# Optimization experiments

Measured on AMD Instinct MI355X. Metric: run time of the kernel, lower is better.

Reference implementation:

```python
import jax, jax.numpy as jnp
import numpy as np

B, T, E, H = 4, 2048, 1024, 16
D = E // H  # head_dim = 64
THETA = 10000.0


def setup_inputs() -> dict:
    key = jax.random.key(0)
    ks = jax.random.split(key, 3)
    s = 0.02
    return {
        "x": jax.random.normal(ks[0], (B, T, E), jnp.float32),
        "W_attn": jax.random.normal(ks[1], (E, 3 * E), jnp.float32) * s,
        "b_attn": jnp.zeros((3 * E,), jnp.float32),
        "W_proj": jax.random.normal(ks[2], (E, E), jnp.float32) * s,
        "b_proj": jnp.zeros((E,), jnp.float32),
    }


def _rope(x, position_offset=0):
    # x: (B, H, T, D) -- interleaved even/odd pair rotation, as in apply_rope
    t, d = x.shape[2], x.shape[3]
    pos = jnp.arange(position_offset, position_offset + t, dtype=jnp.float32)
    inv_freq = 1.0 / (THETA ** (jnp.arange(0, d, 2, dtype=jnp.float32) / d))
    freqs = jnp.outer(pos, inv_freq)  # (T, D/2)
    cos = jnp.cos(freqs)[None, None].astype(x.dtype)
    sin = jnp.sin(freqs)[None, None].astype(x.dtype)
    xe = x[..., ::2]
    xo = x[..., 1::2]
    rot = jnp.stack((xe * cos - xo * sin, xe * sin + xo * cos), axis=-1)
    return rot.reshape(x.shape)


def reference(x, W_attn, b_attn, W_proj, b_proj):
    # fused qkv projection
    qkv = x @ W_attn + b_attn  # (B, T, 3E)
    q, k, v = jnp.split(qkv, 3, axis=-1)

    def heads(a):
        return a.reshape(B, T, H, D).transpose(0, 2, 1, 3)  # (B,H,T,D)

    q, k, v = heads(q), heads(k), heads(v)
    q = _rope(q)
    k = _rope(k)

    scores = jnp.einsum('bhqd,bhkd->bhqk', q, k) * (D ** -0.5)  # (B,H,T,T)
    causal = jnp.tril(jnp.ones((T, T), dtype=bool))
    scores = jnp.where(causal[None, None], scores, -jnp.inf)
    weights = jax.nn.softmax(scores, axis=-1)  # dropout p=0 (eval) -> identity

    out = jnp.einsum('bhqk,bhkd->bhqd', weights, v)
    out = out.transpose(0, 2, 1, 3).reshape(B, T, E)
    return out @ W_proj + b_proj
```

## Files before the change

kernel.cpp:

```cpp
#include <hip/hip_runtime.h>
#include <hip/hip_bf16.h>
#include <math.h>

#define TT 2048
#define HH 16

typedef short s16x8 __attribute__((ext_vector_type(8)));
typedef float f32x4 __attribute__((ext_vector_type(4)));

#define F4(p) (*reinterpret_cast<const float4*>(p))

__device__ __forceinline__ void gload16(const void* g, void* l) {
    __builtin_amdgcn_global_load_lds(
        (const __attribute__((address_space(1))) void*)g,
        (__attribute__((address_space(3))) void*)l, 16, 0, 0);
}

__device__ __forceinline__ ushort bf1(float a) {
    __hip_bfloat16 h = __float2bfloat16(a);
    union { __hip_bfloat16 h1; ushort u; } c; c.h1 = h; return c.u;
}
__device__ __forceinline__ uint pack_bf2(float a, float b) {
    __hip_bfloat162 h = __float22bfloat162_rn(make_float2(a, b));
    union { __hip_bfloat162 h2; uint u; } c; c.h2 = h; return c.u;
}

__global__ __launch_bounds__(256) void prep_kernel(
    const float* __restrict__ x, const float* __restrict__ Wa,
    const float* __restrict__ Wp, ushort* __restrict__ xb,
    ushort* __restrict__ wat, ushort* __restrict__ wpt, float2* __restrict__ cs)
{
    __shared__ float tsh[64][65];
    const int blk = blockIdx.x;
    const int tid = threadIdx.x;

    if (blk < 256) {
        int idx = blk * 256 + tid;
        int t = idx >> 5;
        int i = idx & 31;
        double inv_d = exp(((double)(-2 * i) / 64.0) * log(10000.0));
        float invf = (float)inv_d;
        float freq = (float)t * invf;
        double df = (double)freq;
        cs[idx] = make_float2((float)cos(df), (float)sin(df));
    } else if (blk < 4352) {
        size_t i = (size_t)(blk - 256) * 2048 + (size_t)tid * 8;
        float4 a = F4(&x[i]); float4 b = F4(&x[i + 4]);
        s16x8 v;
        v[0] = bf1(a.x); v[1] = bf1(a.y); v[2] = bf1(a.z); v[3] = bf1(a.w);
        v[4] = bf1(b.x); v[5] = bf1(b.y); v[6] = bf1(b.z); v[7] = bf1(b.w);
        *reinterpret_cast<s16x8*>(&xb[i]) = v;
    } else {
        const float* in; ushort* out; int R, C, bx, by;
        if (blk < 5120) { int r = blk - 4352; in = Wa; out = wat; R = 1024; C = 3072; bx = r % 48; by = r / 48; }
        else            { int r = blk - 5120; in = Wp; out = wpt; R = 1024; C = 1024; bx = r & 15; by = r >> 4; }
        int r0 = by * 64, c0 = bx * 64;
        int ix = tid & 15, iy = tid >> 4;
#pragma unroll
        for (int j = 0; j < 4; ++j) {
            float4 v = F4(&in[(size_t)(r0 + iy + j * 16) * C + c0 + ix * 4]);
            tsh[iy + j * 16][ix * 4 + 0] = v.x;
            tsh[iy + j * 16][ix * 4 + 1] = v.y;
            tsh[iy + j * 16][ix * 4 + 2] = v.z;
            tsh[iy + j * 16][ix * 4 + 3] = v.w;
        }
        __syncthreads();
        int oc = tid >> 2, seg = tid & 3;
        s16x8 u0, u1;
#pragma unroll
        for (int i = 0; i < 8; ++i) u0[i] = bf1(tsh[seg * 16 + i][oc]);
#pragma unroll
        for (int i = 0; i < 8; ++i) u1[i] = bf1(tsh[seg * 16 + 8 + i][oc]);
        ushort* dst = &out[(size_t)(c0 + oc) * R + r0 + seg * 16];
        *reinterpret_cast<s16x8*>(dst) = u0;
        *reinterpret_cast<s16x8*>(dst + 8) = u1;
    }
}

__global__ __launch_bounds__(256, 2) void qkv_gemm_kernel(
    const ushort* __restrict__ xb,
    const ushort* __restrict__ wat,
    const float* __restrict__ bias,
    const float2* __restrict__ cs,
    ushort* __restrict__ qg, ushort* __restrict__ kg, ushort* __restrict__ vt)
{
    __shared__ ushort As[2][8192];
    __shared__ ushort Bs[2][8192];

    const int tid = threadIdx.x;
    const int lane = tid & 63, wid = tid >> 6;
    const int lane15 = lane & 15, kgrp = lane >> 4;
    const int wr = wid >> 1, wc = wid & 1;
    const int m0 = blockIdx.y * 128, n0 = blockIdx.x * 128;
    const int swz = (lane15 & 7) << 4;
    const int srcsw = ((lane & 7) ^ ((lane >> 3) & 7)) * 8;
    const int kgrp16 = kgrp * 16;
    const float SCL = 0.125f * 1.44269504088896f;

    f32x4 acc[4][4] = {};

#define STAGE_QKV(bufi, kofs)                                                     \
    do {                                                                          \
        _Pragma("unroll")                                                         \
        for (int i_ = 0; i_ < 4; ++i_) {                                          \
            int c_ = wid * 4 + i_;                                                \
            gload16(xb + (size_t)(m0 + c_ * 8 + (lane >> 3)) * 1024 + (kofs) + srcsw, \
                    &As[bufi][c_ * 512]);                                         \
            gload16(wat + (size_t)(n0 + c_ * 8 + (lane >> 3)) * 1024 + (kofs) + srcsw, \
                    &Bs[bufi][c_ * 512]);                                         \
        }                                                                         \
    } while (0)

    STAGE_QKV(0, 0);
    int buf = 0;
    for (int kt = 0; kt < 16; ++kt) {
        __syncthreads();
        if (kt < 15) STAGE_QKV(buf ^ 1, (kt + 1) * 64);
        const char* Ap = (const char*)As[buf];
        const char* Bp = (const char*)Bs[buf];
#pragma unroll
        for (int ks = 0; ks < 2; ++ks) {
            s16x8 af[4], bfv[4];
            const int kb = (ks * 64 + kgrp16) ^ swz;
#pragma unroll
            for (int f = 0; f < 4; ++f) {
                int row = wr * 64 + f * 16 + lane15;
                af[f] = *reinterpret_cast<const s16x8*>(Ap + row * 128 + kb);
            }
#pragma unroll
            for (int g = 0; g < 4; ++g) {
                int row = wc * 64 + g * 16 + lane15;
                bfv[g] = *reinterpret_cast<const s16x8*>(Bp + row * 128 + kb);
            }
            __builtin_amdgcn_s_setprio(1);
#pragma unroll
            for (int f = 0; f < 4; ++f)
#pragma unroll
                for (int g = 0; g < 4; ++g)
                    acc[f][g] = __builtin_amdgcn_mfma_f32_16x16x32_bf16(
                        af[f], bfv[g], acc[f][g], 0, 0, 0);
            __builtin_amdgcn_s_setprio(0);
        }
        buf ^= 1;
    }

#pragma unroll
    for (int g = 0; g < 4; ++g) {
        const int n = n0 + wc * 64 + g * 16 + lane15;
        const int sec = n >> 10;
        const int e = n & 1023;
        const int hh = e >> 6, d = e & 63;
        const float bsv = bias[n];
#pragma unroll
        for (int f = 0; f < 4; ++f) {
            const int mb = m0 + wr * 64 + f * 16 + kgrp * 4;
            const int bb = mb >> 11;
            const int t0 = mb & 2047;
            if (sec == 2) {
                float v0 = acc[f][g][0] + bsv, v1 = acc[f][g][1] + bsv;
                float v2 = acc[f][g][2] + bsv, v3 = acc[f][g][3] + bsv;
                uint2 u = make_uint2(pack_bf2(v0, v1), pack_bf2(v2, v3));
                *reinterpret_cast<uint2*>(
                    &vt[((size_t)(bb * HH + hh) * 64 + d) * TT + t0]) = u;
            } else {
                ushort* dst = (sec == 0) ? qg : kg;
#pragma unroll
                for (int r = 0; r < 4; ++r) {
                    float v = acc[f][g][r] + bsv;
                    float p = __shfl_xor(v, 1);
                    float2 c2 = cs[(t0 + r) * 32 + (d >> 1)];
                    float rv = (d & 1) ? (p * c2.y + v * c2.x) : (v * c2.x - p * c2.y);
                    if (sec == 0) rv *= SCL;
                    dst[((size_t)(bb * HH + hh) * TT + t0 + r) * 64 + d] = bf1(rv);
                }
            }
        }
    }
#undef STAGE_QKV
}

__global__ __launch_bounds__(512, 6) void flash_kernel(
    const ushort* __restrict__ qg, const ushort* __restrict__ kg,
    const ushort* __restrict__ vt, ushort* __restrict__ aob)
{
    __shared__ ushort K_s[2][4096];
    __shared__ ushort V_s[2][4096];
    __shared__ ushort P_s[8192];

    const int tid = threadIdx.x;
    const int lane = tid & 63, wid = tid >> 6;
    const int lane15 = lane & 15, kgrp = lane >> 4;
    const int j = blockIdx.x;
    const int qt = 15 - (j >> 6);
    const int bh = j & 63;
    const int b = bh >> 4, h = bh & 15;
    const int q0 = qt * 128;
    const int wq = wid * 16;
    const int wq_abs = q0 + wq;
    const int swz = (lane15 & 7) << 4;
    const int srcsw = ((lane & 7) ^ ((lane >> 3) & 7)) * 8;
    const int kgrp16 = kgrp * 16;
    const int nt = 2 * qt + 2;

    const ushort* qp = qg + (size_t)bh * TT * 64;
    const ushort* kp = kg + (size_t)bh * TT * 64;
    const ushort* vp = vt + (size_t)bh * 64 * TT;
    char* Pw = (char*)P_s + wid * 2048;

#define STAGE_KV(bufi, kv0_)                                                      \
    do {                                                                          \
        gload16(kp + (size_t)((kv0_) + wid * 8 + (lane >> 3)) * 64 + srcsw,       \
                &K_s[bufi][wid * 512]);                                           \
        gload16(vp + (size_t)(wid * 8 + (lane >> 3)) * TT + (kv0_) + srcsw,       \
                &V_s[bufi][wid * 512]);                                           \
    } while (0)

    const ushort* qrow = qp + (size_t)(q0 + wq + lane15) * 64 + kgrp * 8;
    s16x8 qfr[2];
    qfr[0] = *reinterpret_cast<const s16x8*>(qrow);
    qfr[1] = *reinterpret_cast<const s16x8*>(qrow + 32);

    STAGE_KV(0, 0);

    f32x4 o[4] = {};
    float mreg = -3.0e38f;
    float lreg = 0.f;

    int buf = 0;
    for (int t = 0; t < nt; ++t) {
        __syncthreads();
        if (t + 1 < nt) STAGE_KV(buf ^ 1, (t + 1) * 64);

        const int kv0 = t * 64;
        if (kv0 <= wq_abs + 15) {
            const char* Kp = (const char*)K_s[buf];
            const char* Vp = (const char*)V_s[buf];

            f32x4 sacc[4] = {};
#pragma unroll
            for (int ks = 0; ks < 2; ++ks) {
                const int kb = (ks * 64 + kgrp16) ^ swz;
                s16x8 ka[4];
#pragma unroll
                for (int kf = 0; kf < 4; ++kf)
                    ka[kf] = *reinterpret_cast<const s16x8*>(Kp + (kf * 16 + lane15) * 128 + kb);
                __builtin_amdgcn_s_setprio(1);
#pragma unroll
                for (int kf = 0; kf < 4; ++kf)
                    sacc[kf] = __builtin_amdgcn_mfma_f32_16x16x32_bf16(
                        ka[kf], qfr[ks], sacc[kf], 0, 0, 0);
                __builtin_amdgcn_s_setprio(0);
            }

            const int qglob = q0 + wq + lane15;
            const bool masked = (kv0 + 63 > wq_abs);
            float mx = -3.0e38f;
            if (masked) {
#pragma unroll
                for (int kf = 0; kf < 4; ++kf)
#pragma unroll
                    for (int r = 0; r < 4; ++r) {
                        int kvg = kv0 + kf * 16 + kgrp * 4 + r;
                        float v = (kvg > qglob) ? -3.0e38f : sacc[kf][r];
                        sacc[kf][r] = v;
                        mx = fmaxf(mx, v);
                    }
            } else {
#pragma unroll
                for (int kf = 0; kf < 4; ++kf)
#pragma unroll
                    for (int r = 0; r < 4; ++r) mx = fmaxf(mx, sacc[kf][r]);
            }
            mx = fmaxf(mx, __shfl_xor(mx, 16));
            mx = fmaxf(mx, __shfl_xor(mx, 32));
            if (!__all(mx <= mreg + 8.f)) {
                const float mnew = fmaxf(mreg, mx);
                const float fs = exp2f(mreg - mnew);
                lreg *= fs;
#pragma unroll
                for (int df = 0; df < 4; ++df) o[df] *= fs;
                mreg = mnew;
            }
            float rsum = 0.f;
#pragma unroll
            for (int kf = 0; kf < 4; ++kf) {
                float p0 = exp2f(sacc[kf][0] - mreg);
                float p1 = exp2f(sacc[kf][1] - mreg);
                float p2 = exp2f(sacc[kf][2] - mreg);
                float p3 = exp2f(sacc[kf][3] - mreg);
                rsum += (p0 + p1) + (p2 + p3);
                uint2 u = make_uint2(pack_bf2(p0, p1), pack_bf2(p2, p3));
                int kvb = (kf * 32 + kgrp * 8) ^ swz;
                *reinterpret_cast<uint2*>(Pw + lane15 * 128 + kvb) = u;
            }
            rsum += __shfl_xor(rsum, 16);
            rsum += __shfl_xor(rsum, 32);
            lreg += rsum;

#pragma unroll
            for (int ks = 0; ks < 2; ++ks) {
                const int kb = (ks * 64 + kgrp16) ^ swz;
                s16x8 va[4], pb;
#pragma unroll
                for (int df = 0; df < 4; ++df)
                    va[df] = *reinterpret_cast<const s16x8*>(Vp + (df * 16 + lane15) * 128 + kb);
                pb = *reinterpret_cast<const s16x8*>(Pw + lane15 * 128 + kb);
                __builtin_amdgcn_s_setprio(1);
#pragma unroll
                for (int df = 0; df < 4; ++df)
                    o[df] = __builtin_amdgcn_mfma_f32_16x16x32_bf16(
                        va[df], pb, o[df], 0, 0, 0);
                __builtin_amdgcn_s_setprio(0);
            }
        }
        buf ^= 1;
    }

    {
        const float inv = 1.0f / lreg;
        const int row = wq + lane15;
#pragma unroll
        for (int df = 0; df < 4; ++df) {
            float p0 = o[df][0] * inv, p1 = o[df][1] * inv;
            float p2 = o[df][2] * inv, p3 = o[df][3] * inv;
            uint2 u = make_uint2(pack_bf2(p0, p1), pack_bf2(p2, p3));
            int db = (df * 32 + kgrp * 8) ^ ((row & 7) << 4);
            *reinterpret_cast<uint2*>((char*)P_s + row * 128 + db) = u;
        }
    }
    __syncthreads();
    {
        const int q = tid >> 2, seg = tid & 3;
        ushort* orow = aob + ((size_t)(b * TT + q0 + q)) * 1024 + h * 64 + seg * 16;
        int p0 = (seg * 32) ^ ((q & 7) << 4);
        int p1 = (seg * 32 + 16) ^ ((q & 7) << 4);
        s16x8 v0 = *reinterpret_cast<const s16x8*>((const char*)P_s + q * 128 + p0);
        s16x8 v1 = *reinterpret_cast<const s16x8*>((const char*)P_s + q * 128 + p1);
        *reinterpret_cast<s16x8*>(orow) = v0;
        *reinterpret_cast<s16x8*>(orow + 8) = v1;
    }
#undef STAGE_KV
}

__global__ __launch_bounds__(256, 2) void proj_gemm_kernel(
    const ushort* __restrict__ ab,
    const ushort* __restrict__ wpt,
    const float* __restrict__ bias,
    float* __restrict__ out)
{
    __shared__ ushort As[2][8192];
    __shared__ ushort Bs[2][8192];

    const int tid = threadIdx.x;
    const int lane = tid & 63, wid = tid >> 6;
    const int lane15 = lane & 15, kgrp = lane >> 4;
    const int wr = wid >> 1, wc = wid & 1;
    const int m0 = blockIdx.y * 128, n0 = blockIdx.x * 128;
    const int swz = (lane15 & 7) << 4;
    const int srcsw = ((lane & 7) ^ ((lane >> 3) & 7)) * 8;
    const int kgrp16 = kgrp * 16;

    f32x4 acc[4][4] = {};

#define STAGE_PRJ(bufi, kofs)                                                     \
    do {                                                                          \
        _Pragma("unroll")                                                         \
        for (int i_ = 0; i_ < 4; ++i_) {                                          \
            int c_ = wid * 4 + i_;                                                \
            gload16(ab + (size_t)(m0 + c_ * 8 + (lane >> 3)) * 1024 + (kofs) + srcsw, \
                    &As[bufi][c_ * 512]);                                         \
            gload16(wpt + (size_t)(n0 + c_ * 8 + (lane >> 3)) * 1024 + (kofs) + srcsw, \
                    &Bs[bufi][c_ * 512]);                                         \
        }                                                                         \
    } while (0)

    STAGE_PRJ(0, 0);
    int buf = 0;
    for (int kt = 0; kt < 16; ++kt) {
        __syncthreads();
        if (kt < 15) STAGE_PRJ(buf ^ 1, (kt + 1) * 64);
        const char* Ap = (const char*)As[buf];
        const char* Bp = (const char*)Bs[buf];
#pragma unroll
        for (int ks = 0; ks < 2; ++ks) {
            s16x8 af[4], bfv[4];
            const int kb = (ks * 64 + kgrp16) ^ swz;
#pragma unroll
            for (int f = 0; f < 4; ++f) {
                int row = wr * 64 + f * 16 + lane15;
                af[f] = *reinterpret_cast<const s16x8*>(Ap + row * 128 + kb);
            }
#pragma unroll
            for (int g = 0; g < 4; ++g) {
                int row = wc * 64 + g * 16 + lane15;
                bfv[g] = *reinterpret_cast<const s16x8*>(Bp + row * 128 + kb);
            }
            __builtin_amdgcn_s_setprio(1);
#pragma unroll
            for (int f = 0; f < 4; ++f)
#pragma unroll
                for (int g = 0; g < 4; ++g)
                    acc[f][g] = __builtin_amdgcn_mfma_f32_16x16x32_bf16(
                        af[f], bfv[g], acc[f][g], 0, 0, 0);
            __builtin_amdgcn_s_setprio(0);
        }
        buf ^= 1;
    }

#pragma unroll
    for (int g = 0; g < 4; ++g) {
        const int n = n0 + wc * 64 + g * 16 + lane15;
        const float bv = bias[n];
#pragma unroll
        for (int f = 0; f < 4; ++f)
#pragma unroll
            for (int r = 0; r < 4; ++r) {
                const int m = m0 + wr * 64 + f * 16 + kgrp * 4 + r;
                out[(size_t)m * 1024 + n] = acc[f][g][r] + bv;
            }
    }
#undef STAGE_PRJ
}

extern "C" void kernel_launch(void* const* d_in, const int* in_sizes, int n_in,
                              void* d_out, int out_size, void* d_ws, size_t ws_size,
                              hipStream_t stream) {
    const float* x  = (const float*)d_in[0];
    const float* Wa = (const float*)d_in[1];
    const float* ba = (const float*)d_in[2];
    const float* Wp = (const float*)d_in[3];
    const float* bp = (const float*)d_in[4];
    float* out = (float*)d_out;

    char* ws = (char*)d_ws;
    ushort* xb  = (ushort*)(ws + 0);
    ushort* wat = (ushort*)(ws + 16777216);
    ushort* wpt = (ushort*)(ws + 23068672);
    ushort* qg  = (ushort*)(ws + 25165824);
    ushort* kg  = (ushort*)(ws + 41943040);
    ushort* vtg = (ushort*)(ws + 58720256);
    ushort* aob = (ushort*)(ws + 75497472);
    float2* cs  = (float2*)(ws + 92274688);

    prep_kernel<<<dim3(5376), dim3(256), 0, stream>>>(x, Wa, Wp, xb, wat, wpt, cs);
    qkv_gemm_kernel<<<dim3(24, 64), dim3(256), 0, stream>>>(xb, wat, ba, cs, qg, kg, vtg);
    flash_kernel<<<dim3(1024), dim3(512), 0, stream>>>(qg, kg, vtg, aob);
    proj_gemm_kernel<<<dim3(8, 64), dim3(256), 0, stream>>>(aob, wpt, bp, out);
}
```

Measured before the change: 270.3 us.

## Compute softmax row sums via MFMA, use raw exp2, remap GEMM blocks per XCD

In the flash kernel, the per-row sum of probabilities is now taken from an extra MFMA against a vector of bf16 ones, replacing the shuffle reductions. The row max is computed with a balanced fmax tree after the masking step, and exp2f is replaced with the raw hardware v_exp_f32 instruction. Both GEMM kernels switch to a 1D grid whose block indices are remapped so consecutive tiles land on the same XCD, which should improve L2 reuse. The ones-MFMA adds matrix work per tile and sums the bf16-rounded probabilities, so the normalisation changes slightly in precision.

```diff
diff --git a/kernel.cpp b/kernel.cpp
--- a/kernel.cpp
+++ b/kernel.cpp
@@ -23,6 +23,14 @@
 __device__ __forceinline__ uint pack_bf2(float a, float b) {
     __hip_bfloat162 h = __float22bfloat162_rn(make_float2(a, b));
     union { __hip_bfloat162 h2; uint u; } c; c.h2 = h; return c.u;
+}
+
+__device__ __forceinline__ float fexp2(float x) {
+#if __has_builtin(__builtin_amdgcn_exp2f)
+    return __builtin_amdgcn_exp2f(x);
+#else
+    float r; asm("v_exp_f32 %0, %1" : "=v"(r) : "v"(x)); return r;
+#endif
 }
 
 __global__ __launch_bounds__(256) void prep_kernel(
@@ -91,7 +99,9 @@
     const int lane = tid & 63, wid = tid >> 6;
     const int lane15 = lane & 15, kgrp = lane >> 4;
     const int wr = wid >> 1, wc = wid & 1;
-    const int m0 = blockIdx.y * 128, n0 = blockIdx.x * 128;
+    const int bid = blockIdx.x;
+    const int sbid = (bid & 7) * 192 + (bid >> 3);
+    const int n0 = (sbid % 24) * 128, m0 = (sbid / 24) * 128;
     const int swz = (lane15 & 7) << 4;
     const int srcsw = ((lane & 7) ^ ((lane >> 3) & 7)) * 8;
     const int kgrp16 = kgrp * 16;
@@ -220,11 +230,14 @@
     qfr[0] = *reinterpret_cast<const s16x8*>(qrow);
     qfr[1] = *reinterpret_cast<const s16x8*>(qrow + 32);
 
+    s16x8 ones;
+#pragma unroll
+    for (int e = 0; e < 8; ++e) ones[e] = (short)0x3F80;
+
     STAGE_KV(0, 0);
 
-    f32x4 o[4] = {};
+    f32x4 o[5] = {};
     float mreg = -3.0e38f;
-    float lreg = 0.f;
 
     int buf = 0;
     for (int t = 0; t < nt; ++t) {
@@ -253,49 +266,41 @@
             }
 
             const int qglob = q0 + wq + lane15;
-            const bool masked = (kv0 + 63 > wq_abs);
-            float mx = -3.0e38f;
-            if (masked) {
+            if (kv0 + 63 > wq_abs) {
 #pragma unroll
                 for (int kf = 0; kf < 4; ++kf)
 #pragma unroll
                     for (int r = 0; r < 4; ++r) {
                         int kvg = kv0 + kf * 16 + kgrp * 4 + r;
-                        float v = (kvg > qglob) ? -3.0e38f : sacc[kf][r];
-                        sacc[kf][r] = v;
-                        mx = fmaxf(mx, v);
+                        if (kvg > qglob) sacc[kf][r] = -3.0e38f;
                     }
-            } else {
-#pragma unroll
-                for (int kf = 0; kf < 4; ++kf)
-#pragma unroll
-                    for (int r = 0; r < 4; ++r) mx = fmaxf(mx, sacc[kf][r]);
-            }
+            }
+            float t0m = fmaxf(fmaxf(sacc[0][0], sacc[0][1]), sacc[0][2]);
+            float t1m = fmaxf(fmaxf(sacc[0][3], sacc[1][0]), sacc[1][1]);
+            float t2m = fmaxf(fmaxf(sacc[1][2], sacc[1][3]), sacc[2][0]);
+            float t3m = fmaxf(fmaxf(sacc[2][1], sacc[2][2]), sacc[2][3]);
+            float t4m = fmaxf(fmaxf(sacc[3][0], sacc[3][1]), sacc[3][2]);
+            float mx = fmaxf(fmaxf(fmaxf(t0m, t1m), fmaxf(t2m, t3m)),
+                             fmaxf(t4m, sacc[3][3]));
             mx = fmaxf(mx, __shfl_xor(mx, 16));
             mx = fmaxf(mx, __shfl_xor(mx, 32));
             if (!__all(mx <= mreg + 8.f)) {
                 const float mnew = fmaxf(mreg, mx);
-                const float fs = exp2f(mreg - mnew);
-                lreg *= fs;
-#pragma unroll
-                for (int df = 0; df < 4; ++df) o[df] *= fs;
+                const float fs = fexp2(mreg - mnew);
+#pragma unroll
+                for (int df = 0; df < 5; ++df) o[df] *= fs;
                 mreg = mnew;
             }
-            float rsum = 0.f;
 #pragma unroll
             for (int kf = 0; kf < 4; ++kf) {
-                float p0 = exp2f(sacc[kf][0] - mreg);
-                float p1 = exp2f(sacc[kf][1] - mreg);
-                float p2 = exp2f(sacc[kf][2] - mreg);
-                float p3 = exp2f(sacc[kf][3] - mreg);
-                rsum += (p0 + p1) + (p2 + p3);
+                float p0 = fexp2(sacc[kf][0] - mreg);
+                float p1 = fexp2(sacc[kf][1] - mreg);
+                float p2 = fexp2(sacc[kf][2] - mreg);
+                float p3 = fexp2(sacc[kf][3] - mreg);
                 uint2 u = make_uint2(pack_bf2(p0, p1), pack_bf2(p2, p3));
                 int kvb = (kf * 32 + kgrp * 8) ^ swz;
                 *reinterpret_cast<uint2*>(Pw + lane15 * 128 + kvb) = u;
             }
-            rsum += __shfl_xor(rsum, 16);
-            rsum += __shfl_xor(rsum, 32);
-            lreg += rsum;
 
 #pragma unroll
             for (int ks = 0; ks < 2; ++ks) {
@@ -310,6 +315,8 @@
                 for (int df = 0; df < 4; ++df)
                     o[df] = __builtin_amdgcn_mfma_f32_16x16x32_bf16(
                         va[df], pb, o[df], 0, 0, 0);
+                o[4] = __builtin_amdgcn_mfma_f32_16x16x32_bf16(
+                    ones, pb, o[4], 0, 0, 0);
                 __builtin_amdgcn_s_setprio(0);
             }
         }
@@ -317,7 +324,7 @@
     }
 
     {
-        const float inv = 1.0f / lreg;
+        const float inv = 1.0f / o[4][0];
         const int row = wq + lane15;
 #pragma unroll
         for (int df = 0; df < 4; ++df) {
@@ -355,7 +362,9 @@
     const int lane = tid & 63, wid = tid >> 6;
     const int lane15 = lane & 15, kgrp = lane >> 4;
     const int wr = wid >> 1, wc = wid & 1;
-    const int m0 = blockIdx.y * 128, n0 = blockIdx.x * 128;
+    const int bid = blockIdx.x;
+    const int sbid = (bid & 7) * 64 + (bid >> 3);
+    const int n0 = (sbid & 7) * 128, m0 = (sbid >> 3) * 128;
     const int swz = (lane15 & 7) << 4;
     const int srcsw = ((lane & 7) ^ ((lane >> 3) & 7)) * 8;
     const int kgrp16 = kgrp * 16;
@@ -443,7 +452,7 @@
     float2* cs  = (float2*)(ws + 92274688);
 
     prep_kernel<<<dim3(5376), dim3(256), 0, stream>>>(x, Wa, Wp, xb, wat, wpt, cs);
-    qkv_gemm_kernel<<<dim3(24, 64), dim3(256), 0, stream>>>(xb, wat, ba, cs, qg, kg, vtg);
+    qkv_gemm_kernel<<<dim3(1536), dim3(256), 0, stream>>>(xb, wat, ba, cs, qg, kg, vtg);
     flash_kernel<<<dim3(1024), dim3(512), 0, stream>>>(qg, kg, vtg, aob);
-    proj_gemm_kernel<<<dim3(8, 64), dim3(256), 0, stream>>>(aob, wpt, bp, out);
-}
+    proj_gemm_kernel<<<dim3(512), dim3(256), 0, stream>>>(aob, wpt, bp, out);
+}
```

Measured after the change: 258.0 us. 1.05x faster.
